# Optimization experiments

Measured on AMD Instinct MI355X. Metric: run time of the kernel, lower is better.

Reference implementation:

```python
import jax, jax.numpy as jnp
import numpy as np
from jax import lax

N, H, W, C = 64, 256, 256, 16  # NHWC input
O, K = 16, 3                   # out_channels, kern_size


def setup_inputs() -> dict:
    key = jax.random.key(0)
    k_in, k_u, k_v, k_w = jax.random.split(key, 4)
    # glorot_normal std for shape [fan_in, fan_out]-ish 2D weights: sqrt(2/(a+b))
    u = jax.random.normal(k_u, (O, K), dtype=jnp.float32) * np.sqrt(2.0 / (O + K)).astype(np.float32)
    v = jax.random.normal(k_v, (O, K), dtype=jnp.float32) * np.sqrt(2.0 / (O + K)).astype(np.float32)
    w = jax.random.normal(k_w, (O, C), dtype=jnp.float32) * np.sqrt(2.0 / (O + C)).astype(np.float32)
    b = jnp.zeros((O,), dtype=jnp.float32)
    inputs = jax.random.normal(k_in, (N, H, W, C), dtype=jnp.float32)
    return {"inputs": inputs, "u": u, "v": v, "w": w, "b": b}


def reference(inputs, u, v, w, b):
    # CP low-rank kernel construction: kern[i,j,k,l] = v[l,i] * u[l,j] * w[l,k]
    # -> HWIO kernel of shape [K, K, C, O]
    kern = jnp.einsum('lj,lk,li->ijkl', u, w, v)
    out = lax.conv_general_dilated(
        inputs, kern,
        window_strides=(1, 1),
        padding='SAME',
        dimension_numbers=('NHWC', 'HWIO', 'NHWC'),
    )
    return jax.nn.relu(out + b)
```

## Files before the change

kernel.cpp:

```cpp
#include <hip/hip_runtime.h>

#define N_ 64
#define H_ 256
#define W_ 256
#define C_ 16
#define O_ 16

#define CH 16
#define PLANE 258


__device__ __forceinline__ void load_row(const float* __restrict__ base, int r, int x,
                                         float4 pf[4]) {
    const float4* s4 = (const float4*)(base + ((size_t)r * W_ + x) * C_);
    #pragma unroll
    for (int q = 0; q < 4; ++q) pf[q] = s4[q];
}

__device__ __forceinline__ void cmix(const float* __restrict__ w, const float4 pf[4],
                                     float tn[16]) {
    const float iv[16] = {pf[0].x, pf[0].y, pf[0].z, pf[0].w,
                          pf[1].x, pf[1].y, pf[1].z, pf[1].w,
                          pf[2].x, pf[2].y, pf[2].z, pf[2].w,
                          pf[3].x, pf[3].y, pf[3].z, pf[3].w};
    #pragma unroll
    for (int l = 0; l < 16; ++l) {
        float s = 0.f;
        #pragma unroll
        for (int k = 0; k < 16; ++k) s = fmaf(w[l * 16 + k], iv[k], s);
        tn[l] = s;
    }
}

__device__ __forceinline__ void write_t(float4* __restrict__ lds, int slot, int x,
                                        const float tn[16]) {
    #pragma unroll
    for (int q = 0; q < 4; ++q)
        lds[(slot * 4 + q) * PLANE + (x + 1)] =
            make_float4(tn[4 * q], tn[4 * q + 1], tn[4 * q + 2], tn[4 * q + 3]);
}

__device__ __forceinline__ void hrow(const float4* __restrict__ lds, int slot, int x,
                                     const float* __restrict__ u, const float tn[16],
                                     float h[16]) {
    float4 m4[4], p4[4];
    #pragma unroll
    for (int q = 0; q < 4; ++q) {
        m4[q] = lds[(slot * 4 + q) * PLANE + x];
        p4[q] = lds[(slot * 4 + q) * PLANE + x + 2];
    }
    const float tm[16] = {m4[0].x, m4[0].y, m4[0].z, m4[0].w,
                          m4[1].x, m4[1].y, m4[1].z, m4[1].w,
                          m4[2].x, m4[2].y, m4[2].z, m4[2].w,
                          m4[3].x, m4[3].y, m4[3].z, m4[3].w};
    const float tp[16] = {p4[0].x, p4[0].y, p4[0].z, p4[0].w,
                          p4[1].x, p4[1].y, p4[1].z, p4[1].w,
                          p4[2].x, p4[2].y, p4[2].z, p4[2].w,
                          p4[3].x, p4[3].y, p4[3].z, p4[3].w};
    #pragma unroll
    for (int l = 0; l < 16; ++l)
        h[l] = fmaf(u[l * 3 + 0], tm[l],
               fmaf(u[l * 3 + 2], tp[l], u[l * 3 + 1] * tn[l]));
}

__global__ __launch_bounds__(256, 4)
void sep_conv_kernel(const float* __restrict__ in,
                     const float* __restrict__ u,
                     const float* __restrict__ v,
                     const float* __restrict__ w,
                     const float* __restrict__ b,
                     float* __restrict__ out) {
    __shared__ float4 t_lds[2 * 4 * PLANE];

    const int x  = threadIdx.x;
    const int y0 = blockIdx.x * CH;
    const int n  = blockIdx.y;

    const float* inb  = in  + (size_t)n * H_ * W_ * C_;
    float*       outb = out + (size_t)n * H_ * W_ * C_;

    if (x < 16) {
        const int slot = x >> 3, q = (x >> 1) & 3, side = x & 1;
        t_lds[(slot * 4 + q) * PLANE + (side ? PLANE - 1 : 0)] =
            make_float4(0.f, 0.f, 0.f, 0.f);
    }

    float4 pf[4];
    float tn[16], hp[16], hc[16], hn[16];

    const int rm1 = y0 - 1;
    const bool have_m1 = (rm1 >= 0);
    if (have_m1) {
        load_row(inb, rm1, x, pf);
        cmix(w, pf, tn);
    }
    load_row(inb, y0, x, pf);
    if (have_m1) write_t(t_lds, rm1 & 1, x, tn);
    __syncthreads();
    if (have_m1) {
        hrow(t_lds, rm1 & 1, x, u, tn, hp);
    } else {
        #pragma unroll
        for (int l = 0; l < 16; ++l) hp[l] = 0.f;
    }

    cmix(w, pf, tn);
    load_row(inb, y0 + 1, x, pf);
    write_t(t_lds, y0 & 1, x, tn);
    __syncthreads();
    hrow(t_lds, y0 & 1, x, u, tn, hc);

    for (int yy = 0; yy < CH; ++yy) {
        const int y  = y0 + yy;
        const int rn = y + 1;
        if (rn < H_) {
            cmix(w, pf, tn);
            if (yy + 1 < CH && rn + 1 < H_)
                load_row(inb, rn + 1, x, pf);
            write_t(t_lds, rn & 1, x, tn);
            __syncthreads();
            hrow(t_lds, rn & 1, x, u, tn, hn);
        } else {
            #pragma unroll
            for (int l = 0; l < 16; ++l) hn[l] = 0.f;
        }

        float r[16];
        #pragma unroll
        for (int l = 0; l < 16; ++l) {
            float val = fmaf(v[l * 3 + 0], hp[l],
                        fmaf(v[l * 3 + 1], hc[l],
                        fmaf(v[l * 3 + 2], hn[l], b[l])));
            r[l] = fmaxf(val, 0.f);
        }
        float4* o4 = (float4*)(outb + ((size_t)y * W_ + x) * C_);
        o4[0] = make_float4(r[0],  r[1],  r[2],  r[3]);
        o4[1] = make_float4(r[4],  r[5],  r[6],  r[7]);
        o4[2] = make_float4(r[8],  r[9],  r[10], r[11]);
        o4[3] = make_float4(r[12], r[13], r[14], r[15]);

        #pragma unroll
        for (int l = 0; l < 16; ++l) { hp[l] = hc[l]; hc[l] = hn[l]; }
    }
}

extern "C" void kernel_launch(void* const* d_in, const int* in_sizes, int n_in,
                              void* d_out, int out_size, void* d_ws, size_t ws_size,
                              hipStream_t stream) {
    const float* in = (const float*)d_in[0];
    const float* u  = (const float*)d_in[1];
    const float* v  = (const float*)d_in[2];
    const float* w  = (const float*)d_in[3];
    const float* b  = (const float*)d_in[4];
    float* out = (float*)d_out;

    dim3 grid(H_ / CH, N_);
    dim3 block(256);
    sep_conv_kernel<<<grid, block, 0, stream>>>(in, u, v, w, b, out);
}
```

Baseline: 464.5 us.

## Split rows into single-wavefront 64-column strips with halo recompute, drop barriers

Each block is now one 64-lane wavefront covering a 64-pixel strip of a row band, so the LDS exchange of channel-mixed values needs no __syncthreads. Halo columns are recomputed by lanes 0-31, each producing one channel of the two neighbour pixels. This removes block-wide barriers and the double-buffered LDS. In exchange it adds redundant halo loads and dot products, and relies on wavefront-lockstep LDS ordering without any explicit fence. It also quadruples the block count while shrinking each block.

```diff
diff --git a/kernel.cpp b/kernel.cpp
--- a/kernel.cpp
+++ b/kernel.cpp
@@ -6,120 +6,136 @@
 #define C_ 16
 #define O_ 16
 
+#define SW 64
 #define CH 16
-#define PLANE 258
+#define NCOL 66
 
 
-__device__ __forceinline__ void load_row(const float* __restrict__ base, int r, int x,
-                                         float4 pf[4]) {
-    const float4* s4 = (const float4*)(base + ((size_t)r * W_ + x) * C_);
-    #pragma unroll
-    for (int q = 0; q < 4; ++q) pf[q] = s4[q];
-}
-
-__device__ __forceinline__ void cmix(const float* __restrict__ w, const float4 pf[4],
-                                     float tn[16]) {
-    const float iv[16] = {pf[0].x, pf[0].y, pf[0].z, pf[0].w,
-                          pf[1].x, pf[1].y, pf[1].z, pf[1].w,
-                          pf[2].x, pf[2].y, pf[2].z, pf[2].w,
-                          pf[3].x, pf[3].y, pf[3].z, pf[3].w};
-    #pragma unroll
-    for (int l = 0; l < 16; ++l) {
-        float s = 0.f;
-        #pragma unroll
-        for (int k = 0; k < 16; ++k) s = fmaf(w[l * 16 + k], iv[k], s);
-        tn[l] = s;
-    }
-}
-
-__device__ __forceinline__ void write_t(float4* __restrict__ lds, int slot, int x,
-                                        const float tn[16]) {
-    #pragma unroll
-    for (int q = 0; q < 4; ++q)
-        lds[(slot * 4 + q) * PLANE + (x + 1)] =
-            make_float4(tn[4 * q], tn[4 * q + 1], tn[4 * q + 2], tn[4 * q + 3]);
-}
-
-__device__ __forceinline__ void hrow(const float4* __restrict__ lds, int slot, int x,
-                                     const float* __restrict__ u, const float tn[16],
-                                     float h[16]) {
-    float4 m4[4], p4[4];
-    #pragma unroll
-    for (int q = 0; q < 4; ++q) {
-        m4[q] = lds[(slot * 4 + q) * PLANE + x];
-        p4[q] = lds[(slot * 4 + q) * PLANE + x + 2];
-    }
-    const float tm[16] = {m4[0].x, m4[0].y, m4[0].z, m4[0].w,
-                          m4[1].x, m4[1].y, m4[1].z, m4[1].w,
-                          m4[2].x, m4[2].y, m4[2].z, m4[2].w,
-                          m4[3].x, m4[3].y, m4[3].z, m4[3].w};
-    const float tp[16] = {p4[0].x, p4[0].y, p4[0].z, p4[0].w,
-                          p4[1].x, p4[1].y, p4[1].z, p4[1].w,
-                          p4[2].x, p4[2].y, p4[2].z, p4[2].w,
-                          p4[3].x, p4[3].y, p4[3].z, p4[3].w};
-    #pragma unroll
-    for (int l = 0; l < 16; ++l)
-        h[l] = fmaf(u[l * 3 + 0], tm[l],
-               fmaf(u[l * 3 + 2], tp[l], u[l * 3 + 1] * tn[l]));
-}
-
-__global__ __launch_bounds__(256, 4)
+__global__ __launch_bounds__(64, 3)
 void sep_conv_kernel(const float* __restrict__ in,
                      const float* __restrict__ u,
                      const float* __restrict__ v,
                      const float* __restrict__ w,
                      const float* __restrict__ b,
                      float* __restrict__ out) {
-    __shared__ float4 t_lds[2 * 4 * PLANE];
+    __shared__ float4 t_lds[4 * NCOL];
 
-    const int x  = threadIdx.x;
-    const int y0 = blockIdx.x * CH;
-    const int n  = blockIdx.y;
+    const int lane = threadIdx.x;
+    const int x0   = blockIdx.x * SW;
+    const int y0   = blockIdx.y * CH;
+    const int n    = blockIdx.z;
+    const int gx   = x0 + lane;
 
     const float* inb  = in  + (size_t)n * H_ * W_ * C_;
     float*       outb = out + (size_t)n * H_ * W_ * C_;
 
-    if (x < 16) {
-        const int slot = x >> 3, q = (x >> 1) & 3, side = x & 1;
-        t_lds[(slot * 4 + q) * PLANE + (side ? PLANE - 1 : 0)] =
-            make_float4(0.f, 0.f, 0.f, 0.f);
+    const int  which = (lane >> 4) & 1;
+    const int  hl    = lane & 15;
+    const int  hx    = which ? (x0 + SW) : (x0 - 1);
+    const bool hval  = (unsigned)hx < (unsigned)W_;
+
+    float4 wh4[4];
+    {
+        const float4* s4 = (const float4*)(w + hl * 16);
+        #pragma unroll
+        for (int q = 0; q < 4; ++q) wh4[q] = s4[q];
     }
 
-    float4 pf[4];
-    float tn[16], hp[16], hc[16], hn[16];
+    float4 pf[4], xh[4];
+    float  tn[16], th;
+    float  hp[16], hc[16], hn[16];
+    #pragma unroll
+    for (int q = 0; q < 4; ++q) xh[q] = make_float4(0.f, 0.f, 0.f, 0.f);
 
-    const int rm1 = y0 - 1;
-    const bool have_m1 = (rm1 >= 0);
-    if (have_m1) {
-        load_row(inb, rm1, x, pf);
-        cmix(w, pf, tn);
-    }
-    load_row(inb, y0, x, pf);
-    if (have_m1) write_t(t_lds, rm1 & 1, x, tn);
-    __syncthreads();
-    if (have_m1) {
-        hrow(t_lds, rm1 & 1, x, u, tn, hp);
+#define LOAD_MAIN(r) {                                                         \
+    const float4* s4_ = (const float4*)(inb + ((size_t)(r) * W_ + gx) * C_);   \
+    pf[0] = s4_[0]; pf[1] = s4_[1]; pf[2] = s4_[2]; pf[3] = s4_[3]; }
+
+#define LOAD_HALO(r) {                                                         \
+    if (hval) {                                                                \
+        const float4* s4_ = (const float4*)(inb + ((size_t)(r) * W_ + hx) * C_);\
+        xh[0] = s4_[0]; xh[1] = s4_[1]; xh[2] = s4_[2]; xh[3] = s4_[3]; } }
+
+#define CMIX_MAIN() {                                                          \
+    const float iv_[16] = {pf[0].x, pf[0].y, pf[0].z, pf[0].w,                 \
+                           pf[1].x, pf[1].y, pf[1].z, pf[1].w,                 \
+                           pf[2].x, pf[2].y, pf[2].z, pf[2].w,                 \
+                           pf[3].x, pf[3].y, pf[3].z, pf[3].w};                \
+    _Pragma("unroll")                                                          \
+    for (int l = 0; l < 16; ++l) {                                             \
+        float s_ = 0.f;                                                        \
+        _Pragma("unroll")                                                      \
+        for (int k = 0; k < 16; ++k) s_ = fmaf(w[l * 16 + k], iv_[k], s_);     \
+        tn[l] = s_;                                                            \
+    } }
+
+#define CMIX_HALO() {                                                          \
+    const float whf_[16] = {wh4[0].x, wh4[0].y, wh4[0].z, wh4[0].w,            \
+                            wh4[1].x, wh4[1].y, wh4[1].z, wh4[1].w,            \
+                            wh4[2].x, wh4[2].y, wh4[2].z, wh4[2].w,            \
+                            wh4[3].x, wh4[3].y, wh4[3].z, wh4[3].w};           \
+    const float xhf_[16] = {xh[0].x, xh[0].y, xh[0].z, xh[0].w,                \
+                            xh[1].x, xh[1].y, xh[1].z, xh[1].w,                \
+                            xh[2].x, xh[2].y, xh[2].z, xh[2].w,                \
+                            xh[3].x, xh[3].y, xh[3].z, xh[3].w};               \
+    th = 0.f;                                                                  \
+    _Pragma("unroll")                                                          \
+    for (int k = 0; k < 16; ++k) th = fmaf(whf_[k], xhf_[k], th); }
+
+#define EXCHANGE_AND_H(hdst) {                                                 \
+    t_lds[0 * NCOL + lane + 1] = make_float4(tn[0],  tn[1],  tn[2],  tn[3]);   \
+    t_lds[1 * NCOL + lane + 1] = make_float4(tn[4],  tn[5],  tn[6],  tn[7]);   \
+    t_lds[2 * NCOL + lane + 1] = make_float4(tn[8],  tn[9],  tn[10], tn[11]);  \
+    t_lds[3 * NCOL + lane + 1] = make_float4(tn[12], tn[13], tn[14], tn[15]);  \
+    if (lane < 32) {                                                           \
+        ((float*)t_lds)[((hl >> 2) * NCOL + (which ? (NCOL - 1) : 0)) * 4 +    \
+                        (hl & 3)] = th;                                        \
+    }                                                                          \
+    float4 m4_[4], p4_[4];                                                     \
+    _Pragma("unroll")                                                          \
+    for (int q = 0; q < 4; ++q) {                                              \
+        m4_[q] = t_lds[q * NCOL + lane];                                       \
+        p4_[q] = t_lds[q * NCOL + lane + 2];                                   \
+    }                                                                          \
+    const float tm_[16] = {m4_[0].x, m4_[0].y, m4_[0].z, m4_[0].w,             \
+                           m4_[1].x, m4_[1].y, m4_[1].z, m4_[1].w,             \
+                           m4_[2].x, m4_[2].y, m4_[2].z, m4_[2].w,             \
+                           m4_[3].x, m4_[3].y, m4_[3].z, m4_[3].w};            \
+    const float tp_[16] = {p4_[0].x, p4_[0].y, p4_[0].z, p4_[0].w,             \
+                           p4_[1].x, p4_[1].y, p4_[1].z, p4_[1].w,             \
+                           p4_[2].x, p4_[2].y, p4_[2].z, p4_[2].w,             \
+                           p4_[3].x, p4_[3].y, p4_[3].z, p4_[3].w};            \
+    _Pragma("unroll")                                                          \
+    for (int l = 0; l < 16; ++l)                                               \
+        hdst[l] = fmaf(u[l * 3 + 0], tm_[l],                                   \
+                  fmaf(u[l * 3 + 2], tp_[l], u[l * 3 + 1] * tn[l])); }
+
+#define PRODUCE(hdst, r_next, do_pref) {                                       \
+    CMIX_MAIN();                                                               \
+    if (do_pref) LOAD_MAIN(r_next);                                            \
+    CMIX_HALO();                                                               \
+    if (do_pref) LOAD_HALO(r_next);                                            \
+    EXCHANGE_AND_H(hdst); }
+
+    if (y0 > 0) {
+        LOAD_MAIN(y0 - 1);
+        LOAD_HALO(y0 - 1);
+        PRODUCE(hp, y0, true);
     } else {
         #pragma unroll
         for (int l = 0; l < 16; ++l) hp[l] = 0.f;
+        LOAD_MAIN(y0);
+        LOAD_HALO(y0);
     }
-
-    cmix(w, pf, tn);
-    load_row(inb, y0 + 1, x, pf);
-    write_t(t_lds, y0 & 1, x, tn);
-    __syncthreads();
-    hrow(t_lds, y0 & 1, x, u, tn, hc);
+    PRODUCE(hc, y0 + 1, true);
 
     for (int yy = 0; yy < CH; ++yy) {
         const int y  = y0 + yy;
         const int rn = y + 1;
         if (rn < H_) {
-            cmix(w, pf, tn);
-            if (yy + 1 < CH && rn + 1 < H_)
-                load_row(inb, rn + 1, x, pf);
-            write_t(t_lds, rn & 1, x, tn);
-            __syncthreads();
-            hrow(t_lds, rn & 1, x, u, tn, hn);
+            const int  rnext = rn + 1;
+            const bool pref  = (yy + 1 < CH) && (rnext < H_);
+            PRODUCE(hn, rnext, pref);
         } else {
             #pragma unroll
             for (int l = 0; l < 16; ++l) hn[l] = 0.f;
@@ -133,7 +149,7 @@
                         fmaf(v[l * 3 + 2], hn[l], b[l])));
             r[l] = fmaxf(val, 0.f);
         }
-        float4* o4 = (float4*)(outb + ((size_t)y * W_ + x) * C_);
+        float4* o4 = (float4*)(outb + ((size_t)y * W_ + gx) * C_);
         o4[0] = make_float4(r[0],  r[1],  r[2],  r[3]);
         o4[1] = make_float4(r[4],  r[5],  r[6],  r[7]);
         o4[2] = make_float4(r[8],  r[9],  r[10], r[11]);
@@ -142,6 +158,13 @@
         #pragma unroll
         for (int l = 0; l < 16; ++l) { hp[l] = hc[l]; hc[l] = hn[l]; }
     }
+
+#undef LOAD_MAIN
+#undef LOAD_HALO
+#undef CMIX_MAIN
+#undef CMIX_HALO
+#undef EXCHANGE_AND_H
+#undef PRODUCE
 }
 
 extern "C" void kernel_launch(void* const* d_in, const int* in_sizes, int n_in,
@@ -154,7 +177,7 @@
     const float* b  = (const float*)d_in[4];
     float* out = (float*)d_out;
 
-    dim3 grid(H_ / CH, N_);
-    dim3 block(256);
+    dim3 grid(W_ / SW, H_ / CH, N_);
+    dim3 block(SW);
     sep_conv_kernel<<<grid, block, 0, stream>>>(in, u, v, w, b, out);
 }
```

After: 473.6 us. About the same (+2.0%).
